# Kernel tuning notes

Measured on AMD Instinct MI355X. Metric: run time of the kernel, lower is better.

The kernel has to match this reference:

```python
import jax, jax.numpy as jnp
from jax import lax
import numpy as np

NEG = -1e30


def setup_inputs() -> dict:
    key = jax.random.key(0)
    k0, k1, k2, k3 = jax.random.split(key, 4)
    B, txt_T, mel_T, n_mel = 32, 256, 2048, 80
    mu_logvar = jax.random.normal(k0, (B, txt_T, 2 * n_mel), jnp.float32)
    melspec = jax.random.normal(k1, (B, n_mel, mel_T), jnp.float32)
    text_lengths = jax.random.randint(k2, (B,), txt_T // 2, txt_T + 1)
    mel_lengths = jax.random.randint(k3, (B,), mel_T // 2, mel_T + 1)
    return dict(mu_logvar=mu_logvar, melspec=melspec,
                text_lengths=text_lengths, mel_lengths=mel_lengths)


def _log_prob_matrix(mu_logvar, melspec):
    # Gaussian log-prob (mean over mel channels), expanded into GEMM form:
    # -0.5/n_mel * sum_c [ (x_c - mu_c)^2 * exp(-logvar_c) + logvar_c ]
    n_mel = melspec.shape[1]
    mu = mu_logvar[..., :n_mel]           # [B, txt_T, C]
    logvar = mu_logvar[..., n_mel:]       # [B, txt_T, C]
    x = jnp.swapaxes(melspec, 1, 2)       # [B, mel_T, C]
    inv_var = jnp.exp(-logvar)
    t1 = jnp.einsum('btc,bjc->bjt', x * x, inv_var)        # sum x^2/var
    t2 = jnp.einsum('btc,bjc->bjt', x, mu * inv_var)       # sum x*mu/var
    t3 = jnp.sum(mu * mu * inv_var, axis=-1)               # [B, txt_T]
    t4 = jnp.sum(logvar, axis=-1)                          # [B, txt_T]
    return -0.5 * (t1 - 2.0 * t2 + (t3 + t4)[:, :, None]) / n_mel  # [B, txt_T, mel_T]


def _mdn_loss(mu_logvar, melspec, text_lengths, mel_lengths):
    log_prob = _log_prob_matrix(mu_logvar, melspec)   # [B, txt_T, mel_T]
    B, txt_T, mel_T = log_prob.shape
    col0 = jnp.full((B, txt_T), NEG, log_prob.dtype).at[:, 0].set(log_prob[:, 0, 0])

    def step(col, lp_t):
        shifted = jnp.concatenate([jnp.full((B, 1), NEG, col.dtype), col[:, :-1]], axis=1)
        new = jnp.logaddexp(col, shifted) + lp_t
        return new, new

    lp_rest = jnp.moveaxis(log_prob[:, :, 1:], 2, 0)  # [mel_T-1, B, txt_T]
    _, cols = lax.scan(step, col0, lp_rest)
    log_alpha = jnp.concatenate([col0[None], cols], axis=0)  # [mel_T, B, txt_T]

    b = jnp.arange(B)
    alpha_last = log_alpha[mel_lengths - 1, b, text_lengths - 1]
    alpha_last = alpha_last / mel_lengths.astype(log_prob.dtype)
    return -alpha_last.mean(), log_prob


def reference(mu_logvar, melspec, text_lengths, mel_lengths):
    mdn_loss, log_prob_matrix = _mdn_loss(mu_logvar, melspec, text_lengths, mel_lengths)
    return mdn_loss, log_prob_matrix
```

## Files before the change

### kernel.cpp

```cpp
#include <hip/hip_runtime.h>
#include <cstddef>
#include <cstdint>

#define NEGV -1e30f

constexpr int B_    = 32;
constexpr int TXT   = 256;
constexpr int MEL   = 2048;
constexpr int NMEL  = 80;

constexpr int NGROUPS = 511;
constexpr int GSTRIDE = 520;

#define INV_LN2 1.4426950408889634f
#define LN2     0.6931471805599453f
#define M_DEAD  (-(1 << 30))

typedef float f32x4 __attribute__((ext_vector_type(4)));
typedef unsigned short u16;
typedef unsigned int   u32;

__device__ __forceinline__ float wave_ror1_f(float x) {
    int xi = __float_as_int(x);
    int r  = __builtin_amdgcn_update_dpp(xi, xi, 0x13C , 0xF, 0xF, false);
    return __int_as_float(r);
}
__device__ __forceinline__ int wave_ror1_i(int x) {
    return __builtin_amdgcn_update_dpp(x, x, 0x13C, 0xF, 0xF, false);
}
__device__ __forceinline__ float exp2_nat(float x) {
#if __has_builtin(__builtin_amdgcn_exp2f)
    return __builtin_amdgcn_exp2f(x);
#else
    float r; asm("v_exp_f32 %0, %1" : "=v"(r) : "v"(x)); return r;
#endif
}
__device__ __forceinline__ float log2_nat(float x) {
#if __has_builtin(__builtin_amdgcn_logf)
    return __builtin_amdgcn_logf(x);
#else
    float r; asm("v_log_f32 %0, %1" : "=v"(r) : "v"(x)); return r;
#endif
}
__device__ __forceinline__ float ldexp_nat(float x, int n) {
#if __has_builtin(__builtin_amdgcn_ldexpf)
    return __builtin_amdgcn_ldexpf(x, n);
#else
    float r; asm("v_ldexp_f32 %0, %1, %2" : "=v"(r) : "v"(x), "v"(n)); return r;
#endif
}

__device__ __forceinline__ u32 f2bf(float x) {
    u32 u = __float_as_uint(x);
    u += 0x7FFFu + ((u >> 16) & 1u);
    return u >> 16;
}
__device__ __forceinline__ f32x4 bf4(uint2 w) {
    f32x4 r;
    r[0] = __uint_as_float(w.x << 16);
    r[1] = __uint_as_float(w.x & 0xFFFF0000u);
    r[2] = __uint_as_float(w.y << 16);
    r[3] = __uint_as_float(w.y & 0xFFFF0000u);
    return r;
}
__device__ __forceinline__ unsigned lds_off(const void* p) {
    return (unsigned)(unsigned long long)
        (const __attribute__((address_space(3))) char*)p;
}

__global__ __launch_bounds__(256) void precompute_kernel(
    const float* __restrict__ mu_logvar,
    float* __restrict__ IV, float* __restrict__ M2, float* __restrict__ S)
{
    const int b = blockIdx.x;
    const int j = threadIdx.x;
    const float* row = mu_logvar + (size_t)(b * TXT + j) * (2 * NMEL);
    float s = 0.f;
    for (int c = 0; c < NMEL; ++c) {
        float mu = row[c];
        float lv = row[NMEL + c];
        float iv = expf(-lv);
        IV[(b * NMEL + c) * TXT + j] = iv;
        M2[(b * NMEL + c) * TXT + j] = 2.0f * mu * iv;
        s += mu * mu * iv + lv;
    }
    S[b * TXT + j] = s;
}

__global__ __launch_bounds__(256) void logprob_kernel(
    const float* __restrict__ mel,
    const float* __restrict__ IV, const float* __restrict__ M2,
    const float* __restrict__ S,
    float* __restrict__ out1,
    u16* __restrict__ lpT,
    int write_lpT)
{
    const int tt0 = blockIdx.x * 128;
    const int j0  = blockIdx.y * 64;
    const int b   = blockIdx.z;
    const int tx  = threadIdx.x & 15;
    const int ty  = threadIdx.x >> 4;

    __shared__ union SM {
        struct { float IV[NMEL][64]; float M2[NMEL][64]; } stage;
        float V[64][132];
    } sm;

    for (int idx = threadIdx.x; idx < NMEL * 64; idx += 256) {
        int c  = idx >> 6;
        int jj = idx & 63;
        sm.stage.IV[c][jj] = IV[(b * NMEL + c) * TXT + j0 + jj];
        sm.stage.M2[c][jj] = M2[(b * NMEL + c) * TXT + j0 + jj];
    }
    __syncthreads();

    float acc[4][8];
#pragma unroll
    for (int a = 0; a < 4; ++a)
#pragma unroll
        for (int d = 0; d < 8; ++d) acc[a][d] = 0.f;

    const float* melb = mel + (size_t)b * NMEL * MEL + tt0 + tx;

#pragma unroll 2
    for (int c = 0; c < NMEL; ++c) {
        float x[8];
#pragma unroll
        for (int d = 0; d < 8; ++d) x[d] = melb[(size_t)c * MEL + 16 * d];
        float4 iv = *(const float4*)&sm.stage.IV[c][ty * 4];
        float4 m2 = *(const float4*)&sm.stage.M2[c][ty * 4];
        float ivr[4] = {iv.x, iv.y, iv.z, iv.w};
        float m2r[4] = {m2.x, m2.y, m2.z, m2.w};
#pragma unroll
        for (int a = 0; a < 4; ++a) {
#pragma unroll
            for (int d = 0; d < 8; ++d) {
                float tmp = fmaf(ivr[a], x[d], -m2r[a]);
                acc[a][d] = fmaf(tmp, x[d], acc[a][d]);
            }
        }
    }

    const float c0 = -0.5f / (float)NMEL;
    float4 sj = *(const float4*)&S[b * TXT + j0 + ty * 4];
    float sjr[4] = {sj.x, sj.y, sj.z, sj.w};

    __syncthreads();
#pragma unroll
    for (int a = 0; a < 4; ++a) {
        const int jl = ty * 4 + a;
#pragma unroll
        for (int d = 0; d < 8; ++d) {
            sm.V[jl][tx + 16 * d] = c0 * (acc[a][d] + sjr[a]);
        }
    }
    __syncthreads();

    const int tid = threadIdx.x;

    {
        const int t4 = (tid & 31) * 4;
        const int jb = tid >> 5;
#pragma unroll
        for (int k = 0; k < 8; ++k) {
            const int jl = jb + 8 * k;
            float4 v = *(const float4*)&sm.V[jl][t4];
            *(float4*)&out1[(size_t)(b * TXT + j0 + jl) * MEL + tt0 + t4] = v;
        }
    }

    if (write_lpT) {
        const int j4 = (tid & 15) * 4;
        const int tb = tid >> 4;
#pragma unroll
        for (int k = 0; k < 8; ++k) {
            const int tl = tb + 16 * k;
            float pa = exp2_nat(sm.V[j4 + 0][tl] * INV_LN2);
            float pb = exp2_nat(sm.V[j4 + 1][tl] * INV_LN2);
            float pc = exp2_nat(sm.V[j4 + 2][tl] * INV_LN2);
            float pd = exp2_nat(sm.V[j4 + 3][tl] * INV_LN2);
            uint2 w;
            w.x = f2bf(pa) | (f2bf(pb) << 16);
            w.y = f2bf(pc) | (f2bf(pd) << 16);
            *(uint2*)&lpT[((size_t)b * MEL + tt0 + tl) * TXT + j0 + j4] = w;
        }
    }
}

__global__ __launch_bounds__(256) void coeff_kernel(
    const u16* __restrict__ lpT, u16* __restrict__ coef)
{
    const int c = blockIdx.x;
    const int b = blockIdx.y;
    const int j = threadIdx.x;

    __shared__ float sp[32][256];
    const int r0 = 32 * c + 1;
    const u32* src32 = (const u32*)(lpT + (size_t)b * MEL * TXT);
    for (int idx = threadIdx.x; idx < 32 * 128; idx += 256) {
        int row = idx >> 7;
        int col = idx & 127;
        u32 w = src32[(size_t)(r0 + row) * 128 + col];
        sp[row][2 * col]     = __uint_as_float(w << 16);
        sp[row][2 * col + 1] = __uint_as_float(w & 0xFFFF0000u);
    }
    __syncthreads();

    const int jm1 = (j >= 1) ? j - 1 : 0;
    const int jm2 = (j >= 2) ? j - 2 : 0;
    const int jm3 = (j >= 3) ? j - 3 : 0;

#pragma unroll 2
    for (int gi = 0; gi < 8; ++gi) {
        int g = 8 * c + gi;
        if (g >= NGROUPS) break;
        const float* P1 = sp[4 * gi + 0];
        const float* P2 = sp[4 * gi + 1];
        const float* P3 = sp[4 * gi + 2];
        const float* P4 = sp[4 * gi + 3];
        float p1_0 = P1[j], p1_1 = P1[jm1], p1_2 = P1[jm2], p1_3 = P1[jm3];
        float p2_0 = P2[j], p2_1 = P2[jm1], p2_2 = P2[jm2];
        float p3_0 = P3[j], p3_1 = P3[jm1];
        float p4_0 = P4[j];
        float A0 = p2_0 * p1_0, A1 = p2_0 * (p1_0 + p1_1), A2 = p2_0 * p1_1;
        float B0 = p2_1 * p1_1, B1 = p2_1 * (p1_1 + p1_2), B2 = p2_1 * p1_2;
        float D0 = p2_2 * p1_2, D1 = p2_2 * (p1_2 + p1_3), D2 = p2_2 * p1_3;
        float E0 = p3_0 * A0, E1 = p3_0 * (A1 + B0), E2 = p3_0 * (A2 + B1), E3 = p3_0 * B2;
        float F0 = p3_1 * B0, F1 = p3_1 * (B1 + D0), F2 = p3_1 * (B2 + D1), F3 = p3_1 * D2;
        u16* dst = coef + (((size_t)b * GSTRIDE + g) * 5) * 256 + j;
        dst[0]    = (u16)f2bf(p4_0 * E0);
        dst[256]  = (u16)f2bf(p4_0 * (E1 + F0));
        dst[512]  = (u16)f2bf(p4_0 * (E2 + F1));
        dst[768]  = (u16)f2bf(p4_0 * (E3 + F2));
        dst[1024] = (u16)f2bf(p4_0 * F3);
    }
}

__global__ __launch_bounds__(64, 1) void dp_super_kernel(
    const u16* __restrict__ lpT,
    const u16* __restrict__ coef,
    const int* __restrict__ tlen, const int* __restrict__ mlen,
    float* __restrict__ alpha)
{
    const int b = blockIdx.x;
    const int l = threadIdx.x;

    const int tl   = tlen[b];
    const int ml   = mlen[b];
    const int tmax = ml - 1;
    const int jt   = tl - 1;
    const float out_scale = LN2 / (float)ml;

    const u16* sbase = lpT  + (size_t)b * MEL * TXT;
    const u16* cb    = coef + (size_t)b * GSTRIDE * 5 * 256;
    const bool z = (l == 0);

    __shared__ __align__(16) u16 ring[8][1536];

    f32x4 ld0 = bf4(*(const uint2*)(sbase + l * 4));
    int   ex0 = (int)(__float_as_uint(ld0[0]) >> 23) - 126;
    float q0n = ldexp_nat(ld0[0], -ex0);
    float q0 = z ? q0n : 0.f;
    float q1 = 0.f, q2 = 0.f, q3 = 0.f;
    int   M  = z ? ex0 : M_DEAD;

    if (tmax <= 0) {
        if (l == (jt >> 2)) {
            float vv = (jt == 0) ? log2_nat(ld0[0]) : NEGV;
            alpha[b] = vv * out_scale;
        }
        return;
    }

    __builtin_amdgcn_sched_barrier(0);

    const int nss  = tmax >> 2;
    const int tail = tmax & 3;

#define ISSUE_SS(S)                                                           \
    {                                                                         \
        const u16* s_ = cb + (size_t)(S) * 1280;                              \
        u16* d_ = &ring[(S) & 7][0];                                          \
        __builtin_amdgcn_global_load_lds(                                     \
            (const __attribute__((address_space(1))) void*)(s_ + l * 8),      \
            (__attribute__((address_space(3))) void*)d_, 16, 0, 0);           \
        __builtin_amdgcn_global_load_lds(                                     \
            (const __attribute__((address_space(1))) void*)(s_ + 512 + l * 8),\
            (__attribute__((address_space(3))) void*)(d_ + 512), 16, 0, 0);   \
        __builtin_amdgcn_global_load_lds(                                     \
            (const __attribute__((address_space(1))) void*)(s_ + 1024 + l * 8),\
            (__attribute__((address_space(3))) void*)(d_ + 1024), 16, 0, 0);  \
    }

#pragma unroll
    for (int s = 0; s < 7; ++s) ISSUE_SS(s);

    for (int s = 0; s < nss; ++s) {
        ISSUE_SS(s + 7);
        asm volatile("s_waitcnt vmcnt(21)" ::: "memory");
        __builtin_amdgcn_sched_barrier(0);

        const unsigned base = lds_off(&ring[s & 7][0]) + (unsigned)(l * 8);
        uint2 w0, w1, w2, w3, w4;
        asm volatile("ds_read_b64 %0, %1 offset:0"    : "=v"(w0) : "v"(base));
        asm volatile("ds_read_b64 %0, %1 offset:512"  : "=v"(w1) : "v"(base));
        asm volatile("ds_read_b64 %0, %1 offset:1024" : "=v"(w2) : "v"(base));
        asm volatile("ds_read_b64 %0, %1 offset:1536" : "=v"(w3) : "v"(base));
        asm volatile("ds_read_b64 %0, %1 offset:2048" : "=v"(w4) : "v"(base));
        asm volatile("s_waitcnt lgkmcnt(0)");
        __builtin_amdgcn_sched_barrier(0);

        f32x4 C0 = bf4(w0);
        f32x4 C1 = bf4(w1);
        f32x4 C2 = bf4(w2);
        f32x4 C3 = bf4(w3);
        f32x4 C4 = bf4(w4);

        float bq0 = wave_ror1_f(q0), bq1 = wave_ror1_f(q1);
        float bq2 = wave_ror1_f(q2), bq3 = wave_ror1_f(q3);
        int   bM  = wave_ror1_i(M);

        int dq   = z ? (-(1 << 28)) : (bM - M);
        int sin_ = (dq < 0) ? dq  : 0;
        int sown = (dq > 0) ? -dq : 0;
        int mup  = (dq > 0) ? dq  : 0;

        float a0 = ldexp_nat(q0, sown), a1 = ldexp_nat(q1, sown);
        float a2 = ldexp_nat(q2, sown), a3 = ldexp_nat(q3, sown);
        float b0 = ldexp_nat(bq0, sin_), b1 = ldexp_nat(bq1, sin_);
        float b2 = ldexp_nat(bq2, sin_), b3 = ldexp_nat(bq3, sin_);

        float y0 = fmaf(C1[0], b3, fmaf(C2[0], b2, fmaf(C3[0], b1, fmaf(C4[0], b0, C0[0] * a0))));
        float y1 = fmaf(C2[1], b3, fmaf(C3[1], b2, fmaf(C4[1], b1, fmaf(C1[1], a0, C0[1] * a1))));
        float y2 = fmaf(C3[2], b3, fmaf(C4[2], b2, fmaf(C1[2], a1, fmaf(C2[2], a0, C0[2] * a2))));
        float y3 = fmaf(C4[3], b3, fmaf(C1[3], a2, fmaf(C2[3], a1, fmaf(C3[3], a0, C0[3] * a3))));

        float mloc = fmaxf(fmaxf(y0, y1), fmaxf(y2, y3));
        int ex  = (int)(__float_as_uint(mloc) >> 23) - 126;
        int nex = -ex;
        q0 = ldexp_nat(y0, nex); q1 = ldexp_nat(y1, nex);
        q2 = ldexp_nat(y2, nex); q3 = ldexp_nat(y3, nex);
        int Mn = M + mup + ex;
        M = (mloc > 0.f) ? Mn : M_DEAD;
    }

    asm volatile("s_waitcnt vmcnt(0)" ::: "memory");
    __builtin_amdgcn_sched_barrier(0);

    {
        const int t0 = 4 * nss + 1;
        f32x4 pr0 = bf4(*(const uint2*)(sbase + (size_t)(t0 + 0) * TXT + l * 4));
        f32x4 pr1 = bf4(*(const uint2*)(sbase + (size_t)(t0 + 1) * TXT + l * 4));
        f32x4 pr2 = bf4(*(const uint2*)(sbase + (size_t)(t0 + 2) * TXT + l * 4));

#define STEP1(P)                                                   \
    {                                                              \
        float qb = wave_ror1_f(q3);                                \
        int   Mb = wave_ror1_i(M);                                 \
        int dq   = z ? (-(1 << 28)) : (Mb - M);                    \
        int si   = (dq < 0) ? dq  : 0;                             \
        int so   = (dq > 0) ? -dq : 0;                             \
        int mu   = (dq > 0) ? dq  : 0;                             \
        float a0 = ldexp_nat(q0, so), a1 = ldexp_nat(q1, so);      \
        float a2 = ldexp_nat(q2, so), a3 = ldexp_nat(q3, so);      \
        float bb = ldexp_nat(qb, si);                              \
        q0 = (a0 + bb) * (P)[0];                                   \
        q1 = (a1 + a0) * (P)[1];                                   \
        q2 = (a2 + a1) * (P)[2];                                   \
        q3 = (a3 + a2) * (P)[3];                                   \
        M += mu;                                                   \
    }
        if (tail >= 1) STEP1(pr0);
        if (tail >= 2) STEP1(pr1);
        if (tail >= 3) STEP1(pr2);
#undef STEP1
    }
#undef ISSUE_SS

    const int lf = jt >> 2;
    const int ef = jt & 3;
    float v = (ef == 0) ? q0 : (ef == 1) ? q1 : (ef == 2) ? q2 : q3;
    if (l == lf) alpha[b] = (log2_nat(v) + (float)M) * out_scale;
}

__global__ __launch_bounds__(256) void dp_kernel_fallback(
    const float* __restrict__ lp,
    const int* __restrict__ tlen, const int* __restrict__ mlen,
    float* __restrict__ alpha)
{
    const int b    = blockIdx.x;
    const int j    = threadIdx.x;
    const int lane = j & 63;
    const int w    = j >> 6;

    const int tl   = tlen[b];
    const int ml   = mlen[b];
    const int tmax = ml - 1;
    const int jt   = tl - 1;
    const float inv_ml = 1.0f / (float)ml;

    __shared__ float bnd[2][4];
    if (threadIdx.x < 8) bnd[threadIdx.x >> 2][threadIdx.x & 3] = NEGV;
    __syncthreads();

    float cur = (j == 0) ? lp[(size_t)(b * TXT) * MEL] : NEGV;
    if (tmax == 0) {
        if (j == jt) alpha[b] = cur * inv_ml;
        return;
    }
    int p = 0;
    for (int t = 1; t <= tmax; ++t) {
        float lpc = lp[((size_t)(b * TXT + j)) * MEL + t];
        float sh = __shfl_up(cur, 1);
        if (lane == 0) sh = (w > 0) ? bnd[p][w - 1] : NEGV;
        float mx = fmaxf(cur, sh);
        float dd = fminf(cur, sh) - mx;
        float nv = mx + __logf(1.0f + __expf(dd)) + lpc;
        if (lane == 63) bnd[p ^ 1][w] = nv;
        if (t == tmax && j == jt) alpha[b] = nv * inv_ml;
        cur = nv;
        __syncthreads();
        p ^= 1;
    }
}

__global__ void reduce_kernel(const float* __restrict__ alpha, float* __restrict__ out)
{
    const int tid = threadIdx.x;
    float v = (tid < B_) ? alpha[tid] : 0.f;
#pragma unroll
    for (int m = 16; m >= 1; m >>= 1) v += __shfl_xor(v, m);
    if (tid == 0) out[0] = -v / (float)B_;
}

extern "C" void kernel_launch(void* const* d_in, const int* in_sizes, int n_in,
                              void* d_out, int out_size, void* d_ws, size_t ws_size,
                              hipStream_t stream)
{
    const float* mu_logvar = (const float*)d_in[0];
    const float* melspec   = (const float*)d_in[1];
    const int*   tlen      = (const int*)d_in[2];
    const int*   mlen      = (const int*)d_in[3];
    float* out = (float*)d_out;
    float* ws  = (float*)d_ws;

    const size_t IV_OFF    = 0;
    const size_t M2_OFF    = 655360;
    const size_t S_OFF     = 1310720;
    const size_t ALPHA_OFF = 1318912;
    const size_t LPT_OFF   = 1318944;
    const size_t LPT_FLOATS = (size_t)B_ * MEL * TXT / 2;
    const size_t LPT_PAD_F  = 2048;
    const size_t COEF_OFF  = LPT_OFF + LPT_FLOATS + LPT_PAD_F;
    const size_t COEF_FLOATS = (size_t)B_ * GSTRIDE * 5 * 256 / 2;

    float* IV    = ws + IV_OFF;
    float* M2    = ws + M2_OFF;
    float* S     = ws + S_OFF;
    float* alpha = ws + ALPHA_OFF;
    u16*   lpT   = (u16*)(ws + LPT_OFF);
    u16*   coef  = (u16*)(ws + COEF_OFF);

    const bool use_coef = ws_size >= (COEF_OFF + COEF_FLOATS) * sizeof(float);

    precompute_kernel<<<dim3(B_), dim3(256), 0, stream>>>(mu_logvar, IV, M2, S);

    logprob_kernel<<<dim3(MEL / 128, TXT / 64, B_), dim3(256), 0, stream>>>(
        melspec, IV, M2, S, out + 1, lpT, use_coef ? 1 : 0);

    if (use_coef) {
        coeff_kernel<<<dim3(64, B_), dim3(256), 0, stream>>>(lpT, coef);
        dp_super_kernel<<<dim3(B_), dim3(64), 0, stream>>>(lpT, coef, tlen, mlen, alpha);
    } else {
        dp_kernel_fallback<<<dim3(B_), dim3(256), 0, stream>>>(out + 1, tlen, mlen, alpha);
    }

    reduce_kernel<<<dim3(1), dim3(64), 0, stream>>>(alpha, out);
}
```

Baseline: 301.1 us.

## Double-buffer LDS reads in DP loop and vectorize mel loads in GEMM

The DP scan loop is unrolled by two with A/B register sets, so the LDS reads for the next superstep are issued before the current superstep's arithmetic. This hides LDS latency on the serial recurrence, and the vmcnt thresholds are retuned to match. Separately, the log-prob GEMM now has each thread load 8 contiguous mel values with two float4 loads instead of 8 strided scalar loads, and the LDS staging writes change to match. The new mapping may cause LDS bank conflicts on the V writes, and it raises register use in the DP kernel.

Result: no change. 305.2 us (+1.3%).

```diff
diff --git a/kernel.cpp b/kernel.cpp
--- a/kernel.cpp
+++ b/kernel.cpp
@@ -120,13 +120,13 @@
 #pragma unroll
         for (int d = 0; d < 8; ++d) acc[a][d] = 0.f;
 
-    const float* melb = mel + (size_t)b * NMEL * MEL + tt0 + tx;
+    const float* melb = mel + (size_t)b * NMEL * MEL + tt0 + tx * 8;
 
 #pragma unroll 2
     for (int c = 0; c < NMEL; ++c) {
-        float x[8];
-#pragma unroll
-        for (int d = 0; d < 8; ++d) x[d] = melb[(size_t)c * MEL + 16 * d];
+        float4 xa = *(const float4*)&melb[(size_t)c * MEL];
+        float4 xb = *(const float4*)&melb[(size_t)c * MEL + 4];
+        float x[8] = {xa.x, xa.y, xa.z, xa.w, xb.x, xb.y, xb.z, xb.w};
         float4 iv = *(const float4*)&sm.stage.IV[c][ty * 4];
         float4 m2 = *(const float4*)&sm.stage.M2[c][ty * 4];
         float ivr[4] = {iv.x, iv.y, iv.z, iv.w};
@@ -151,7 +151,7 @@
         const int jl = ty * 4 + a;
 #pragma unroll
         for (int d = 0; d < 8; ++d) {
-            sm.V[jl][tx + 16 * d] = c0 * (acc[a][d] + sjr[a]);
+            sm.V[jl][tx * 8 + d] = c0 * (acc[a][d] + sjr[a]);
         }
     }
     __syncthreads();
@@ -292,59 +292,86 @@
             (__attribute__((address_space(3))) void*)(d_ + 1024), 16, 0, 0);  \
     }
 
-#pragma unroll
-    for (int s = 0; s < 7; ++s) ISSUE_SS(s);
-
-    for (int s = 0; s < nss; ++s) {
+#define DS_READ5(W0, W1, W2, W3, W4, BASE)                                    \
+    asm volatile("ds_read_b64 %0, %1 offset:0"    : "=v"(W0) : "v"(BASE));    \
+    asm volatile("ds_read_b64 %0, %1 offset:512"  : "=v"(W1) : "v"(BASE));    \
+    asm volatile("ds_read_b64 %0, %1 offset:1024" : "=v"(W2) : "v"(BASE));    \
+    asm volatile("ds_read_b64 %0, %1 offset:1536" : "=v"(W3) : "v"(BASE));    \
+    asm volatile("ds_read_b64 %0, %1 offset:2048" : "=v"(W4) : "v"(BASE));
+
+#define SUPERSTEP(W0, W1, W2, W3, W4)                                         \
+    {                                                                         \
+        f32x4 C0 = bf4(W0);                                                   \
+        f32x4 C1 = bf4(W1);                                                   \
+        f32x4 C2 = bf4(W2);                                                   \
+        f32x4 C3 = bf4(W3);                                                   \
+        f32x4 C4 = bf4(W4);                                                   \
+        float bq0 = wave_ror1_f(q0), bq1 = wave_ror1_f(q1);                   \
+        float bq2 = wave_ror1_f(q2), bq3 = wave_ror1_f(q3);                   \
+        int   bM  = wave_ror1_i(M);                                           \
+        int dq   = z ? (-(1 << 28)) : (bM - M);                               \
+        int sin_ = (dq < 0) ? dq  : 0;                                        \
+        int sown = (dq > 0) ? -dq : 0;                                        \
+        int mup  = (dq > 0) ? dq  : 0;                                        \
+        float a0 = ldexp_nat(q0, sown), a1 = ldexp_nat(q1, sown);             \
+        float a2 = ldexp_nat(q2, sown), a3 = ldexp_nat(q3, sown);             \
+        float b0 = ldexp_nat(bq0, sin_), b1 = ldexp_nat(bq1, sin_);           \
+        float b2 = ldexp_nat(bq2, sin_), b3 = ldexp_nat(bq3, sin_);           \
+        float y0 = fmaf(C1[0], b3, fmaf(C2[0], b2, fmaf(C3[0], b1, fmaf(C4[0], b0, C0[0] * a0)))); \
+        float y1 = fmaf(C2[1], b3, fmaf(C3[1], b2, fmaf(C4[1], b1, fmaf(C1[1], a0, C0[1] * a1)))); \
+        float y2 = fmaf(C3[2], b3, fmaf(C4[2], b2, fmaf(C1[2], a1, fmaf(C2[2], a0, C0[2] * a2)))); \
+        float y3 = fmaf(C4[3], b3, fmaf(C1[3], a2, fmaf(C2[3], a1, fmaf(C3[3], a0, C0[3] * a3)))); \
+        float mloc = fmaxf(fmaxf(y0, y1), fmaxf(y2, y3));                     \
+        int ex  = (int)(__float_as_uint(mloc) >> 23) - 126;                   \
+        int nex = -ex;                                                        \
+        q0 = ldexp_nat(y0, nex); q1 = ldexp_nat(y1, nex);                     \
+        q2 = ldexp_nat(y2, nex); q3 = ldexp_nat(y3, nex);                     \
+        int Mn = M + mup + ex;                                                \
+        M = (mloc > 0.f) ? Mn : M_DEAD;                                       \
+    }
+
+#pragma unroll
+    for (int sp = 0; sp < 7; ++sp) ISSUE_SS(sp);
+
+    asm volatile("s_waitcnt vmcnt(15)" ::: "memory");
+    __builtin_amdgcn_sched_barrier(0);
+    uint2 A0, A1, A2, A3, A4, Bb0, Bb1, Bb2, Bb3, Bb4;
+    {
+        const unsigned baseA = lds_off(&ring[0][0]) + (unsigned)(l * 8);
+        DS_READ5(A0, A1, A2, A3, A4, baseA);
+    }
+
+    int s = 0;
+    for (; s + 1 < nss; s += 2) {
         ISSUE_SS(s + 7);
-        asm volatile("s_waitcnt vmcnt(21)" ::: "memory");
+        asm volatile("s_waitcnt vmcnt(18)" ::: "memory");
         __builtin_amdgcn_sched_barrier(0);
-
-        const unsigned base = lds_off(&ring[s & 7][0]) + (unsigned)(l * 8);
-        uint2 w0, w1, w2, w3, w4;
-        asm volatile("ds_read_b64 %0, %1 offset:0"    : "=v"(w0) : "v"(base));
-        asm volatile("ds_read_b64 %0, %1 offset:512"  : "=v"(w1) : "v"(base));
-        asm volatile("ds_read_b64 %0, %1 offset:1024" : "=v"(w2) : "v"(base));
-        asm volatile("ds_read_b64 %0, %1 offset:1536" : "=v"(w3) : "v"(base));
-        asm volatile("ds_read_b64 %0, %1 offset:2048" : "=v"(w4) : "v"(base));
+        {
+            const unsigned nb = lds_off(&ring[(s + 1) & 7][0]) + (unsigned)(l * 8);
+            DS_READ5(Bb0, Bb1, Bb2, Bb3, Bb4, nb);
+        }
+        asm volatile("s_waitcnt lgkmcnt(5)");
+        __builtin_amdgcn_sched_barrier(0);
+        SUPERSTEP(A0, A1, A2, A3, A4);
+
+        ISSUE_SS(s + 8);
+        asm volatile("s_waitcnt vmcnt(18)" ::: "memory");
+        __builtin_amdgcn_sched_barrier(0);
+        {
+            const unsigned na = lds_off(&ring[(s + 2) & 7][0]) + (unsigned)(l * 8);
+            DS_READ5(A0, A1, A2, A3, A4, na);
+        }
+        asm volatile("s_waitcnt lgkmcnt(5)");
+        __builtin_amdgcn_sched_barrier(0);
+        SUPERSTEP(Bb0, Bb1, Bb2, Bb3, Bb4);
+    }
+    if (s < nss) {
         asm volatile("s_waitcnt lgkmcnt(0)");
         __builtin_amdgcn_sched_barrier(0);
-
-        f32x4 C0 = bf4(w0);
-        f32x4 C1 = bf4(w1);
-        f32x4 C2 = bf4(w2);
-        f32x4 C3 = bf4(w3);
-        f32x4 C4 = bf4(w4);
-
-        float bq0 = wave_ror1_f(q0), bq1 = wave_ror1_f(q1);
-        float bq2 = wave_ror1_f(q2), bq3 = wave_ror1_f(q3);
-        int   bM  = wave_ror1_i(M);
-
-        int dq   = z ? (-(1 << 28)) : (bM - M);
-        int sin_ = (dq < 0) ? dq  : 0;
-        int sown = (dq > 0) ? -dq : 0;
-        int mup  = (dq > 0) ? dq  : 0;
-
-        float a0 = ldexp_nat(q0, sown), a1 = ldexp_nat(q1, sown);
-        float a2 = ldexp_nat(q2, sown), a3 = ldexp_nat(q3, sown);
-        float b0 = ldexp_nat(bq0, sin_), b1 = ldexp_nat(bq1, sin_);
-        float b2 = ldexp_nat(bq2, sin_), b3 = ldexp_nat(bq3, sin_);
-
-        float y0 = fmaf(C1[0], b3, fmaf(C2[0], b2, fmaf(C3[0], b1, fmaf(C4[0], b0, C0[0] * a0))));
-        float y1 = fmaf(C2[1], b3, fmaf(C3[1], b2, fmaf(C4[1], b1, fmaf(C1[1], a0, C0[1] * a1))));
-        float y2 = fmaf(C3[2], b3, fmaf(C4[2], b2, fmaf(C1[2], a1, fmaf(C2[2], a0, C0[2] * a2))));
-        float y3 = fmaf(C4[3], b3, fmaf(C1[3], a2, fmaf(C2[3], a1, fmaf(C3[3], a0, C0[3] * a3))));
-
-        float mloc = fmaxf(fmaxf(y0, y1), fmaxf(y2, y3));
-        int ex  = (int)(__float_as_uint(mloc) >> 23) - 126;
-        int nex = -ex;
-        q0 = ldexp_nat(y0, nex); q1 = ldexp_nat(y1, nex);
-        q2 = ldexp_nat(y2, nex); q3 = ldexp_nat(y3, nex);
-        int Mn = M + mup + ex;
-        M = (mloc > 0.f) ? Mn : M_DEAD;
-    }
-
-    asm volatile("s_waitcnt vmcnt(0)" ::: "memory");
+        SUPERSTEP(A0, A1, A2, A3, A4);
+    }
+
+    asm volatile("s_waitcnt vmcnt(0) lgkmcnt(0)" ::: "memory");
     __builtin_amdgcn_sched_barrier(0);
 
     {
@@ -375,6 +402,8 @@
         if (tail >= 3) STEP1(pr2);
 #undef STEP1
     }
+#undef SUPERSTEP
+#undef DS_READ5
 #undef ISSUE_SS
 
     const int lf = jt >> 2;
```
